# Kernel optimization log

Hardware: AMD Instinct MI355X
Metric: run time of the kernel (lower is better)

Reference implementation:

```python
import jax, jax.numpy as jnp
import numpy as np


def setup_inputs() -> dict:
    key = jax.random.key(0)
    k1, k2, k3, k4 = jax.random.split(key, 4)
    B, A, C = 16, 65536, 21  # batch, anchors, num_classes+1 (20 fg classes + background)
    loc_preds = jax.random.normal(k1, (B, A, 4), dtype=jnp.float32)
    loc_targets = jax.random.normal(k2, (B, A, 4), dtype=jnp.float32)
    cls_preds = jax.random.normal(k3, (B, A, C), dtype=jnp.float32)
    # -1 = ignore, 0 = background/negative, 1..20 = positive classes
    cls_targets = jax.random.randint(k4, (B, A), -1, C)
    pos = cls_targets > 0
    return {
        "loc_preds": loc_preds,
        "loc_targets": loc_targets,
        "cls_preds": cls_preds,
        "cls_targets": cls_targets,
        "pos": pos,
        "verbose": 0,
    }


def reference(loc_preds, loc_targets, cls_preds, cls_targets, pos, verbose):
    eps = 1e-7
    num_pos = jnp.sum(pos).astype(loc_preds.dtype)

    # smooth L1 over positive anchors (sum reduction, beta=1), mask instead of gather
    posf = pos[..., None].astype(loc_preds.dtype)          # [B, A, 1]
    d = loc_preds - loc_targets
    ad = jnp.abs(d)
    sl1 = jnp.where(ad < 1.0, 0.5 * d * d, ad - 0.5)
    loc_loss = jnp.sum(sl1 * posf)

    # focal loss over non-ignored anchors (cls_targets > -1)
    pos_neg = (cls_targets > -1)[..., None].astype(cls_preds.dtype)  # [B, A, 1]
    C = cls_preds.shape[-1]
    y = jax.nn.one_hot(cls_targets, C, dtype=cls_preds.dtype)  # -1 -> all zeros
    p = jax.nn.softmax(cls_preds, axis=-1)
    p = jnp.clip(p, eps, 1.0 - eps)
    fl = -y * jnp.log(p) * (1.0 - p) ** 2
    cls_loss = jnp.sum(fl * pos_neg)

    return (loc_loss + cls_loss) / num_pos
```

## Files before the change

kernel.cpp:

```cpp
#include <hip/hip_runtime.h>
#include <stdint.h>

#define NCLS 21
#define BLK 256
#define APT 2
#define SPAN (BLK * APT)
#define CLS_ROW_BYTES (NCLS * 4)
#define CLS_TILE_BYTES (SPAN * CLS_ROW_BYTES)
#define NCHUNK (CLS_TILE_BYTES / 1024)

typedef __attribute__((address_space(3))) void       lds_void_t;
typedef __attribute__((address_space(1))) const void gbl_void_t;

__device__ __forceinline__ float fmax4(const float4& v) {
    return fmaxf(fmaxf(v.x, v.y), fmaxf(v.z, v.w));
}
__device__ __forceinline__ float4 fmax44(const float4& a, const float4& b) {
    return make_float4(fmaxf(a.x, b.x), fmaxf(a.y, b.y),
                       fmaxf(a.z, b.z), fmaxf(a.w, b.w));
}

__device__ __forceinline__ float focal_regs(
    int t, const float4& c0, const float4& c1, const float4& c2,
    const float4& c3, const float4& c4, float c20)
{
    float m = fmaxf(fmax4(fmax44(fmax44(c0, c1), fmax44(c2, c3))),
                    fmaxf(fmax4(c4), c20));
    float s = 0.0f, et = 0.0f;
#define FSTEP(val, idx) { float e = __expf((val) - m); s += e; et = (t == (idx)) ? e : et; }
    FSTEP(c0.x, 0)  FSTEP(c0.y, 1)  FSTEP(c0.z, 2)  FSTEP(c0.w, 3)
    FSTEP(c1.x, 4)  FSTEP(c1.y, 5)  FSTEP(c1.z, 6)  FSTEP(c1.w, 7)
    FSTEP(c2.x, 8)  FSTEP(c2.y, 9)  FSTEP(c2.z, 10) FSTEP(c2.w, 11)
    FSTEP(c3.x, 12) FSTEP(c3.y, 13) FSTEP(c3.z, 14) FSTEP(c3.w, 15)
    FSTEP(c4.x, 16) FSTEP(c4.y, 17) FSTEP(c4.z, 18) FSTEP(c4.w, 19)
    FSTEP(c20,  20)
#undef FSTEP
    float pt = et / s;
    pt = fminf(fmaxf(pt, 1e-7f), 1.0f - 1e-7f);
    float om = 1.0f - pt;
    return -__logf(pt) * om * om;
}

__device__ __forceinline__ float focal_lds(int t, const float* __restrict__ row)
{
    float4 c0  = make_float4(row[0],  row[1],  row[2],  row[3]);
    float4 c1  = make_float4(row[4],  row[5],  row[6],  row[7]);
    float4 c2  = make_float4(row[8],  row[9],  row[10], row[11]);
    float4 c3  = make_float4(row[12], row[13], row[14], row[15]);
    float4 c4  = make_float4(row[16], row[17], row[18], row[19]);
    float  c20 = row[20];
    return focal_regs(t, c0, c1, c2, c3, c4, c20);
}

__device__ __forceinline__ float smooth_l1(const float4& lp, const float4& lt) {
    float d0 = lp.x - lt.x, d1 = lp.y - lt.y, d2 = lp.z - lt.z, d3 = lp.w - lt.w;
    float a0 = fabsf(d0), a1 = fabsf(d1), a2 = fabsf(d2), a3 = fabsf(d3);
    float s = 0.0f;
    s += (a0 < 1.0f) ? 0.5f * d0 * d0 : a0 - 0.5f;
    s += (a1 < 1.0f) ? 0.5f * d1 * d1 : a1 - 0.5f;
    s += (a2 < 1.0f) ? 0.5f * d2 * d2 : a2 - 0.5f;
    s += (a3 < 1.0f) ? 0.5f * d3 * d3 : a3 - 0.5f;
    return s;
}

__global__ __launch_bounds__(BLK) void focal_main(
    const float* __restrict__ loc_p,
    const float* __restrict__ loc_t,
    const float* __restrict__ cls_p,
    const int*   __restrict__ cls_t,
    float2* __restrict__ partials,
    int n_anchors)
{
    __shared__ float cls_s[SPAN * NCLS];
    __shared__ float redL[4], redP[4];

    const int tid  = threadIdx.x;
    const int wave = tid >> 6;
    const int lane = tid & 63;
    const long long blk0       = (long long)blockIdx.x * SPAN;
    const long long base_byte  = blk0 * CLS_ROW_BYTES;
    const long long total_byte = (long long)n_anchors * CLS_ROW_BYTES;

    {
        const char* g = (const char*)cls_p + base_byte + (long long)lane * 16;
        char*       l = (char*)cls_s;
        for (int c = wave; c < NCHUNK; c += BLK / 64) {
            const long long gb = base_byte + (long long)c * 1024 + lane * 16;
            if (gb + 16 <= total_byte) {
                __builtin_amdgcn_global_load_lds(
                    (gbl_void_t*)(g + (long long)c * 1024),
                    (lds_void_t*)(l + c * 1024),
                    16, 0, 0);
            } else if (gb < total_byte) {
                for (long long b = gb; b < total_byte; b += 4)
                    cls_s[(b - base_byte) >> 2] = cls_p[b >> 2];
            }
        }
    }

    const long long a0 = blk0 + tid;
    const long long a1 = a0 + BLK;
    const bool v0 = (a0 < n_anchors), v1 = (a1 < n_anchors);

    int t0 = -1, t1 = -1;
    float4 lp0, lt0, lp1, lt1;
    if (v0) {
        t0  = cls_t[a0];
        lp0 = ((const float4*)loc_p)[a0];
        lt0 = ((const float4*)loc_t)[a0];
    }
    if (v1) {
        t1  = cls_t[a1];
        lp1 = ((const float4*)loc_p)[a1];
        lt1 = ((const float4*)loc_t)[a1];
    }

    asm volatile("s_waitcnt vmcnt(0)" ::: "memory");
    __syncthreads();

    float acc = 0.0f, npos = 0.0f;
    if (v0) {
        if (t0 > 0)  { acc += smooth_l1(lp0, lt0); npos += 1.0f; }
        if (t0 >= 0) acc += focal_lds(t0, cls_s + tid * NCLS);
    }
    if (v1) {
        if (t1 > 0)  { acc += smooth_l1(lp1, lt1); npos += 1.0f; }
        if (t1 >= 0) acc += focal_lds(t1, cls_s + (tid + BLK) * NCLS);
    }

    #pragma unroll
    for (int off = 32; off > 0; off >>= 1) {
        acc  += __shfl_down(acc,  off, 64);
        npos += __shfl_down(npos, off, 64);
    }
    if (lane == 0) { redL[wave] = acc; redP[wave] = npos; }
    __syncthreads();
    if (tid == 0)
        partials[blockIdx.x] = make_float2(redL[0] + redL[1] + redL[2] + redL[3],
                                           redP[0] + redP[1] + redP[2] + redP[3]);
}

#define RBLK 1024
__global__ __launch_bounds__(RBLK) void focal_reduce(
    const float2* __restrict__ partials, float* __restrict__ out, int npart)
{
    __shared__ float red[32];
    float L = 0.0f, P = 0.0f;
    for (int i = threadIdx.x; i < npart; i += RBLK) {
        float2 v = partials[i];
        L += v.x; P += v.y;
    }
    #pragma unroll
    for (int off = 32; off > 0; off >>= 1) {
        L += __shfl_down(L, off, 64);
        P += __shfl_down(P, off, 64);
    }
    const int wave = threadIdx.x >> 6, lane = threadIdx.x & 63;
    if (lane == 0) { red[wave * 2] = L; red[wave * 2 + 1] = P; }
    __syncthreads();
    if (threadIdx.x == 0) {
        float Ls = 0.0f, Ps = 0.0f;
        #pragma unroll
        for (int w = 0; w < RBLK / 64; ++w) { Ls += red[w * 2]; Ps += red[w * 2 + 1]; }
        out[0] = Ls / Ps;
    }
}

extern "C" void kernel_launch(void* const* d_in, const int* in_sizes, int n_in,
                              void* d_out, int out_size, void* d_ws, size_t ws_size,
                              hipStream_t stream)
{
    const float* loc_p = (const float*)d_in[0];
    const float* loc_t = (const float*)d_in[1];
    const float* cls_p = (const float*)d_in[2];
    const int*   cls_t = (const int*)d_in[3];
    float*  out = (float*)d_out;
    float2* ws  = (float2*)d_ws;

    const int n_anchors = in_sizes[3];
    const int blocks = (n_anchors + SPAN - 1) / SPAN;

    focal_main<<<blocks, BLK, 0, stream>>>(loc_p, loc_t, cls_p, cls_t, ws, n_anchors);
    focal_reduce<<<1, RBLK, 0, stream>>>(ws, out, blocks);
}
```

Measured before the change: 167.8 us.

## Stage class tiles per wave with split waitcnt to overlap compute

Each wave now stages its own two 64-anchor class tiles into LDS with global_load_lds and waits only on the first tile (vmcnt(9)) before computing it, so the second tile's load overlaps the first tile's focal math. The block-wide __syncthreads before compute and all the bounds checks are removed. A remainder kernel handles leftover anchors. This relies on the vmcnt count being correct and on LDS writes from global_load_lds being visible within the wave without a barrier.

Result: no change. 168.4 us (+0.3%).

```diff
diff --git a/kernel.cpp b/kernel.cpp
--- a/kernel.cpp
+++ b/kernel.cpp
@@ -2,15 +2,18 @@
 #include <stdint.h>
 
 #define NCLS 21
-#define BLK 256
-#define APT 2
-#define SPAN (BLK * APT)
+#define BLK  256
+#define SPAN 512
+#define TILE 64
+#define TILE_BYTES (TILE * NCLS * 4)
 #define CLS_ROW_BYTES (NCLS * 4)
-#define CLS_TILE_BYTES (SPAN * CLS_ROW_BYTES)
-#define NCHUNK (CLS_TILE_BYTES / 1024)
 
 typedef __attribute__((address_space(3))) void       lds_void_t;
 typedef __attribute__((address_space(1))) const void gbl_void_t;
+
+__device__ __forceinline__ float4 load_f4u(const float* p) {
+    float4 v; __builtin_memcpy(&v, p, 16); return v;
+}
 
 __device__ __forceinline__ float fmax4(const float4& v) {
     return fmaxf(fmaxf(v.x, v.y), fmaxf(v.z, v.w));
@@ -63,70 +66,62 @@
     return s;
 }
 
+__device__ __forceinline__ void stage_tile(const char* gsrc, char* lbuf, int lane)
+{
+    #pragma unroll
+    for (int c = 0; c < 5; ++c)
+        __builtin_amdgcn_global_load_lds(
+            (gbl_void_t*)(gsrc + c * 1024 + lane * 16),
+            (lds_void_t*)(lbuf + c * 1024), 16, 0, 0);
+    __builtin_amdgcn_global_load_lds(
+        (gbl_void_t*)(gsrc + 5120 + lane * 4),
+        (lds_void_t*)(lbuf + 5120), 4, 0, 0);
+}
+
 __global__ __launch_bounds__(BLK) void focal_main(
     const float* __restrict__ loc_p,
     const float* __restrict__ loc_t,
     const float* __restrict__ cls_p,
     const int*   __restrict__ cls_t,
-    float2* __restrict__ partials,
-    int n_anchors)
-{
-    __shared__ float cls_s[SPAN * NCLS];
+    float2* __restrict__ partials)
+{
+    __shared__ float cls_s[4][2][TILE * NCLS];
     __shared__ float redL[4], redP[4];
 
     const int tid  = threadIdx.x;
     const int wave = tid >> 6;
     const int lane = tid & 63;
-    const long long blk0       = (long long)blockIdx.x * SPAN;
-    const long long base_byte  = blk0 * CLS_ROW_BYTES;
-    const long long total_byte = (long long)n_anchors * CLS_ROW_BYTES;
-
-    {
-        const char* g = (const char*)cls_p + base_byte + (long long)lane * 16;
-        char*       l = (char*)cls_s;
-        for (int c = wave; c < NCHUNK; c += BLK / 64) {
-            const long long gb = base_byte + (long long)c * 1024 + lane * 16;
-            if (gb + 16 <= total_byte) {
-                __builtin_amdgcn_global_load_lds(
-                    (gbl_void_t*)(g + (long long)c * 1024),
-                    (lds_void_t*)(l + c * 1024),
-                    16, 0, 0);
-            } else if (gb < total_byte) {
-                for (long long b = gb; b < total_byte; b += 4)
-                    cls_s[(b - base_byte) >> 2] = cls_p[b >> 2];
-            }
-        }
-    }
-
-    const long long a0 = blk0 + tid;
-    const long long a1 = a0 + BLK;
-    const bool v0 = (a0 < n_anchors), v1 = (a1 < n_anchors);
-
-    int t0 = -1, t1 = -1;
-    float4 lp0, lt0, lp1, lt1;
-    if (v0) {
-        t0  = cls_t[a0];
-        lp0 = ((const float4*)loc_p)[a0];
-        lt0 = ((const float4*)loc_t)[a0];
-    }
-    if (v1) {
-        t1  = cls_t[a1];
-        lp1 = ((const float4*)loc_p)[a1];
-        lt1 = ((const float4*)loc_t)[a1];
-    }
+    const long long blk0 = (long long)blockIdx.x * SPAN;
+    const long long t0a  = blk0 + (long long)wave * TILE;
+    const long long t1a  = t0a + 256;
+
+    char* b0 = (char*)&cls_s[wave][0][0];
+    char* b1 = (char*)&cls_s[wave][1][0];
+
+    stage_tile((const char*)cls_p + t0a * CLS_ROW_BYTES, b0, lane);
+
+    const long long a0 = t0a + lane;
+    const int    t0  = cls_t[a0];
+    const float4 lp0 = ((const float4*)loc_p)[a0];
+    const float4 lt0 = ((const float4*)loc_t)[a0];
+
+    stage_tile((const char*)cls_p + t1a * CLS_ROW_BYTES, b1, lane);
+
+    const long long a1 = t1a + lane;
+    const int    t1  = cls_t[a1];
+    const float4 lp1 = ((const float4*)loc_p)[a1];
+    const float4 lt1 = ((const float4*)loc_t)[a1];
+
+    asm volatile("s_waitcnt vmcnt(9)" ::: "memory");
+
+    float acc = 0.0f, npos = 0.0f;
+    if (t0 > 0)  { acc += smooth_l1(lp0, lt0); npos += 1.0f; }
+    if (t0 >= 0) acc += focal_lds(t0, (const float*)b0 + lane * NCLS);
 
     asm volatile("s_waitcnt vmcnt(0)" ::: "memory");
-    __syncthreads();
-
-    float acc = 0.0f, npos = 0.0f;
-    if (v0) {
-        if (t0 > 0)  { acc += smooth_l1(lp0, lt0); npos += 1.0f; }
-        if (t0 >= 0) acc += focal_lds(t0, cls_s + tid * NCLS);
-    }
-    if (v1) {
-        if (t1 > 0)  { acc += smooth_l1(lp1, lt1); npos += 1.0f; }
-        if (t1 >= 0) acc += focal_lds(t1, cls_s + (tid + BLK) * NCLS);
-    }
+
+    if (t1 > 0)  { acc += smooth_l1(lp1, lt1); npos += 1.0f; }
+    if (t1 >= 0) acc += focal_lds(t1, (const float*)b1 + lane * NCLS);
 
     #pragma unroll
     for (int off = 32; off > 0; off >>= 1) {
@@ -138,6 +133,42 @@
     if (tid == 0)
         partials[blockIdx.x] = make_float2(redL[0] + redL[1] + redL[2] + redL[3],
                                            redP[0] + redP[1] + redP[2] + redP[3]);
+}
+
+__global__ __launch_bounds__(BLK) void focal_tail(
+    const float* __restrict__ loc_p,
+    const float* __restrict__ loc_t,
+    const float* __restrict__ cls_p,
+    const int*   __restrict__ cls_t,
+    float2* __restrict__ partials,
+    int start, int n_anchors)
+{
+    __shared__ float redL[4], redP[4];
+    const int tid = threadIdx.x, wave = tid >> 6, lane = tid & 63;
+    float acc = 0.0f, npos = 0.0f;
+    for (long long a = start + tid; a < n_anchors; a += BLK) {
+        const int t = cls_t[a];
+        if (t > 0) {
+            float4 lp = ((const float4*)loc_p)[a];
+            float4 lt = ((const float4*)loc_t)[a];
+            acc += smooth_l1(lp, lt); npos += 1.0f;
+        }
+        if (t >= 0) {
+            const float* g = cls_p + a * NCLS;
+            acc += focal_regs(t, load_f4u(g), load_f4u(g + 4), load_f4u(g + 8),
+                              load_f4u(g + 12), load_f4u(g + 16), g[20]);
+        }
+    }
+    #pragma unroll
+    for (int off = 32; off > 0; off >>= 1) {
+        acc  += __shfl_down(acc,  off, 64);
+        npos += __shfl_down(npos, off, 64);
+    }
+    if (lane == 0) { redL[wave] = acc; redP[wave] = npos; }
+    __syncthreads();
+    if (tid == 0)
+        partials[0] = make_float2(redL[0] + redL[1] + redL[2] + redL[3],
+                                  redP[0] + redP[1] + redP[2] + redP[3]);
 }
 
 #define RBLK 1024
@@ -178,8 +209,13 @@
     float2* ws  = (float2*)d_ws;
 
     const int n_anchors = in_sizes[3];
-    const int blocks = (n_anchors + SPAN - 1) / SPAN;
-
-    focal_main<<<blocks, BLK, 0, stream>>>(loc_p, loc_t, cls_p, cls_t, ws, n_anchors);
-    focal_reduce<<<1, RBLK, 0, stream>>>(ws, out, blocks);
-}
+    const int nfull = n_anchors / SPAN;
+    const int rem   = n_anchors - nfull * SPAN;
+
+    if (nfull > 0)
+        focal_main<<<nfull, BLK, 0, stream>>>(loc_p, loc_t, cls_p, cls_t, ws);
+    if (rem > 0)
+        focal_tail<<<1, BLK, 0, stream>>>(loc_p, loc_t, cls_p, cls_t,
+                                          ws + nfull, nfull * SPAN, n_anchors);
+    focal_reduce<<<1, RBLK, 0, stream>>>(ws, out, nfull + (rem ? 1 : 0));
+}
```
